# Kernel optimization log

Hardware: AMD Instinct MI355X
Metric: run time of the kernel (lower is better)

Reference implementation:

```python
import jax, jax.numpy as jnp
import numpy as np

B, S, D_MODEL, H = 4, 1024, 1024, 16
HD = D_MODEL // H  # head_dim = 64


def setup_inputs() -> dict:
    key = jax.random.key(0)
    ks = jax.random.split(key, 12)
    sd = 1.0 / np.sqrt(D_MODEL)
    return {
        "x": jax.random.normal(ks[0], (B, S, D_MODEL), dtype=jnp.float32),
        "Wq": jax.random.normal(ks[1], (D_MODEL, D_MODEL), dtype=jnp.float32) * sd,
        "bq": jnp.zeros((D_MODEL,), dtype=jnp.float32),
        "Wk": jax.random.normal(ks[2], (D_MODEL, D_MODEL), dtype=jnp.float32) * sd,
        "bk": jnp.zeros((D_MODEL,), dtype=jnp.float32),
        "Wv": jax.random.normal(ks[3], (D_MODEL, D_MODEL), dtype=jnp.float32) * sd,
        "bv": jnp.zeros((D_MODEL,), dtype=jnp.float32),
        "W1": jax.random.normal(ks[4], (2 * D_MODEL, D_MODEL), dtype=jnp.float32) * sd,
        "b1": jnp.zeros((2 * D_MODEL,), dtype=jnp.float32),
        "W2": jax.random.normal(ks[5], (D_MODEL, 2 * D_MODEL), dtype=jnp.float32) * (1.0 / np.sqrt(2 * D_MODEL)),
        "b2": jnp.zeros((D_MODEL,), dtype=jnp.float32),
        "mask": jnp.ones((B, S, S), dtype=jnp.int32),
    }


def reference(x, Wq, bq, Wk, bk, Wv, bv, W1, b1, W2, b2, mask):
    # QKV projections (torch Linear: y = x @ W.T + b), split into heads -> [B,H,S,HD]
    def proj(W, b):
        return (x @ W.T + b).reshape(B, S, H, HD).transpose(0, 2, 1, 3)

    q = proj(Wq, bq)
    k = proj(Wk, bk)
    v = proj(Wv, bv)

    scores = jnp.einsum("bhqd,bhkd->bhqk", q, k) / jnp.sqrt(jnp.float32(HD))
    # mask [B,S,S] broadcast over heads (original does unsqueeze(1).repeat)
    scores = jnp.where(mask[:, None, :, :] == 0, jnp.float32(-1e8), scores)
    probs = jax.nn.softmax(scores, axis=-1)
    ctx = jnp.einsum("bhqk,bhkd->bhqd", probs, v)
    ctx = ctx.transpose(0, 2, 1, 3).reshape(B, S, D_MODEL)

    # out-projection MLP: Linear(d, 2d) -> ReLU -> Linear(2d, d)
    h = jax.nn.relu(ctx @ W1.T + b1)
    return h @ W2.T + b2
```

## Files before the change

### kernel.cpp

```cpp
#include <hip/hip_runtime.h>
#include <hip/hip_bf16.h>
#include <stdint.h>


#define B_ 4
#define S_ 1024
#define DM_ 1024
#define H_ 16
#define HD_ 64

typedef __attribute__((ext_vector_type(8))) short short8;
typedef __attribute__((ext_vector_type(4))) float f32x4;
typedef __attribute__((ext_vector_type(4))) unsigned short ushort4v;

#define GLB_AS(p) ((const __attribute__((address_space(1))) void*)(p))
#define LDS_AS(p) ((__attribute__((address_space(3))) void*)(p))

__device__ __forceinline__ void async_load16(const void* g, void* l) {
  __builtin_amdgcn_global_load_lds(GLB_AS(g), LDS_AS(l), 16, 0, 0);
}

__device__ __forceinline__ unsigned short f2bf(float x) {
  union { float f; unsigned int u; } v; v.f = x;
  unsigned int r = v.u + 0x7fffu + ((v.u >> 16) & 1u);
  return (unsigned short)(r >> 16);
}

#define QSCALE 0.18033688011112042f

struct PrepArgs {
  const float* src[6];
  unsigned short* dst[6];
  int n4[6];
  const int* mask;
  unsigned long long* bits;
  unsigned int* rowflag;
  const float* bq;
  const float* bk;
  const float* bv;
  float* cb;
};

__global__ void prep_kernel(PrepArgs a) {
  const int seg = blockIdx.y;
  if (seg < 6) {
    const int n4 = a.n4[seg];
    const f32x4* __restrict__ src = (const f32x4*)a.src[seg];
    ushort4v* __restrict__ dst = (ushort4v*)a.dst[seg];
    for (int i = blockIdx.x * blockDim.x + threadIdx.x; i < n4;
         i += gridDim.x * blockDim.x) {
      f32x4 v = src[i];
      ushort4v o;
      o[0] = f2bf(v[0]); o[1] = f2bf(v[1]); o[2] = f2bf(v[2]); o[3] = f2bf(v[3]);
      dst[i] = o;
    }
  } else if (seg == 6) {
    const int wave = threadIdx.x >> 6;
    const int lane = threadIdx.x & 63;
    const int row = blockIdx.x * 4 + wave;
    const int4* mr = (const int4*)(a.mask + (size_t)row * S_) + lane * 4;
    unsigned int chunk = 0;
#pragma unroll
    for (int t = 0; t < 4; ++t) {
      const int4 v = mr[t];
      chunk |= (v.x != 0 ? 1u : 0u) << (4 * t + 0);
      chunk |= (v.y != 0 ? 1u : 0u) << (4 * t + 1);
      chunk |= (v.z != 0 ? 1u : 0u) << (4 * t + 2);
      chunk |= (v.w != 0 ? 1u : 0u) << (4 * t + 3);
    }
    unsigned long long v64 = (unsigned long long)chunk << (16 * (lane & 3));
    v64 |= __shfl_xor(v64, 1);
    v64 |= __shfl_xor(v64, 2);
    if ((lane & 3) == 0) a.bits[(size_t)row * 16 + (lane >> 2)] = v64;
    const bool all1 = (__ballot(chunk == 0xffffu) == ~0ull);
    if (lane == 0) a.rowflag[row] = all1 ? 1u : 0u;
  } else {
    const int i = blockIdx.x * 256 + threadIdx.x;
    if (i < 3072) {
      const float* src = (i < 1024) ? a.bq : (i < 2048) ? a.bk : a.bv;
      a.cb[i] = src[i & 1023];
    }
  }
}

enum { EPI_QKV = 0, EPI_RELU_BF16 = 2, EPI_F32 = 3, EPI_PARTIAL = 4 };

template <int EPI>
__global__ __launch_bounds__(256, 3) void gemm_bt(
    const unsigned short* __restrict__ A, const unsigned short* __restrict__ Bt,
    const float* __restrict__ bias, void* __restrict__ Cp,
    unsigned short* __restrict__ Vt, int M, int N, int K, int Kld) {
  __shared__ __align__(16) unsigned short smem[128 * 136];
  unsigned short* sA = smem;
  unsigned short* sB = smem + 128 * 64;

  const int tid = threadIdx.x;
  const int lane = tid & 63;
  const int wave = tid >> 6;
  const int quad = lane >> 4;
  const int l15 = lane & 15;
  const int swzb = l15 & 7;
  const int m0 = blockIdx.y * 128;
  const int n0 = blockIdx.x * 128;
  const int wm = (wave >> 1) * 64;
  const int wn = (wave & 1) * 64;
  const int kz = blockIdx.z * K;

  f32x4 acc[4][4];
#pragma unroll
  for (int i = 0; i < 4; ++i)
#pragma unroll
    for (int j = 0; j < 4; ++j) acc[i][j] = (f32x4){0.f, 0.f, 0.f, 0.f};

  const int srow = tid >> 3;
  const int scol = ((tid & 7) ^ (srow & 7)) * 8;
  const unsigned short* gA = A + (size_t)(m0 + srow) * Kld + kz + scol;
  const unsigned short* gB = Bt + (size_t)(n0 + srow) * Kld + kz + scol;
  unsigned short* lA = sA + tid * 8;
  unsigned short* lB = sB + tid * 8;

  for (int k0 = 0; k0 < K; k0 += 64) {
    __syncthreads();
#pragma unroll
    for (int st = 0; st < 4; ++st) {
      async_load16(gA + (size_t)(st * 32) * Kld + k0, lA + st * 2048);
      async_load16(gB + (size_t)(st * 32) * Kld + k0, lB + st * 2048);
    }
    __syncthreads();

#pragma unroll
    for (int ks = 0; ks < 2; ++ks) {
      short8 af[4], bfr[4];
#pragma unroll
      for (int t = 0; t < 4; ++t) {
        const int cg = ((ks * 4 + quad) ^ swzb) * 8;
        af[t] = *(const short8*)(sA + (wm + t * 16 + l15) * 64 + cg);
        bfr[t] = *(const short8*)(sB + (wn + t * 16 + l15) * 64 + cg);
      }
#pragma unroll
      for (int mt = 0; mt < 4; ++mt)
#pragma unroll
        for (int nt = 0; nt < 4; ++nt)
          acc[mt][nt] = __builtin_amdgcn_mfma_f32_16x16x32_bf16(
              af[mt], bfr[nt], acc[mt][nt], 0, 0, 0);
    }
  }

  if (EPI == EPI_QKV && n0 >= 2048) {
    __syncthreads();
#pragma unroll
    for (int nt = 0; nt < 4; ++nt) {
      const int col = n0 + wn + nt * 16 + l15;
      const float bv = bias[col];
#pragma unroll
      for (int mt = 0; mt < 4; ++mt)
#pragma unroll
        for (int r = 0; r < 4; ++r)
          smem[(wn + nt * 16 + l15) * 136 + wm + mt * 16 + quad * 4 + r] =
              f2bf(acc[mt][nt][r] + bv);
    }
    __syncthreads();
    const int vc0 = n0 - 2048;
    const int bb = m0 >> 10;
    const int s0 = m0 & 1023;
#pragma unroll
    for (int i = 0; i < 8; ++i) {
      const int c = i * 16 + (tid >> 4);
      const int tc = tid & 15;
      const short8 val = *(const short8*)(smem + c * 136 + tc * 8);
      const int ch = vc0 + c;
      const int hh = ch >> 6, dd = ch & 63;
      *(short8*)(Vt + ((size_t)(bb * 16 + hh) * HD_ + dd) * S_ + s0 + tc * 8) =
          val;
    }
    return;
  }

#pragma unroll
  for (int nt = 0; nt < 4; ++nt) {
    const int col = n0 + wn + nt * 16 + l15;
    const float bv = (EPI == EPI_PARTIAL) ? 0.f : bias[col];
    const float scl = (EPI == EPI_QKV && col < 1024) ? QSCALE : 1.0f;
#pragma unroll
    for (int mt = 0; mt < 4; ++mt) {
#pragma unroll
      for (int r = 0; r < 4; ++r) {
        const int row = m0 + wm + mt * 16 + quad * 4 + r;
        float v = acc[mt][nt][r] + bv;
        if (EPI == EPI_F32) {
          ((float*)Cp)[(size_t)row * N + col] = v;
        } else if (EPI == EPI_PARTIAL) {
          ((float*)Cp)[(size_t)blockIdx.z * M * N + (size_t)row * N + col] = v;
        } else if (EPI == EPI_RELU_BF16) {
          ((unsigned short*)Cp)[(size_t)row * N + col] = f2bf(fmaxf(v, 0.f));
        } else {
          ((unsigned short*)Cp)[(size_t)row * N + col] = f2bf(v * scl);
        }
      }
    }
  }
}

__global__ __launch_bounds__(256, 3) void flash_attn(
    const unsigned short* __restrict__ Cqkv, const unsigned short* __restrict__ Vt,
    const unsigned long long* __restrict__ mbits,
    const unsigned int* __restrict__ mrowflag,
    unsigned short* __restrict__ ctx) {
  __shared__ unsigned short sK[128 * 64];
  __shared__ unsigned short sV[64 * 128];
  __shared__ unsigned short spb[4][16 * 136];

  const int tid = threadIdx.x;
  const int wave = tid >> 6;
  const int lane = tid & 63;
  const int quad = lane >> 4;
  const int l15 = lane & 15;
  const int bh = blockIdx.x;
  const int b = bh >> 4;
  const int h = bh & 15;
  const int qbase = blockIdx.y * 128 + wave * 32;

  const unsigned short* Qb = Cqkv + (size_t)(b * S_) * 3072 + h * HD_;
  const unsigned short* Kb = Cqkv + (size_t)(b * S_) * 3072 + DM_ + h * HD_;
  const unsigned short* Vb = Vt + (size_t)bh * HD_ * S_;
  unsigned short* pbuf = spb[wave];

  bool mask_all_ones;
  {
    unsigned int f = mrowflag[b * S_ + qbase + (lane & 31)];
    mask_all_ones = (__ballot(f != 0) == ~0ull);
  }

  short8 qf[2][2];
#pragma unroll
  for (int u = 0; u < 2; ++u)
#pragma unroll
    for (int ks = 0; ks < 2; ++ks)
      qf[u][ks] = *(const short8*)(Qb + (size_t)(qbase + u * 16 + l15) * 3072 +
                                   ks * 32 + quad * 8);

  f32x4 o[2][4];
#pragma unroll
  for (int u = 0; u < 2; ++u)
#pragma unroll
    for (int i = 0; i < 4; ++i) o[u][i] = (f32x4){0.f, 0.f, 0.f, 0.f};
  float lsum[2][4] = {{0.f, 0.f, 0.f, 0.f}, {0.f, 0.f, 0.f, 0.f}};

  for (int kt = 0; kt < S_ / 128; ++kt) {
    const int kbase = kt * 128;

    __syncthreads();
#pragma unroll
    for (int st = 0; st < 4; ++st) {
      const int j = st * 256 + tid;
      const int r = j >> 3, c = j & 7;
      async_load16(Kb + (size_t)(kbase + r) * 3072 + ((c ^ (r & 7)) * 8),
                   sK + j * 8);
    }
#pragma unroll
    for (int st = 0; st < 4; ++st) {
      const int j = st * 256 + tid;
      const int d = j >> 4, c = j & 15;
      async_load16(Vb + (size_t)d * S_ + kbase + ((c ^ (d & 15)) * 8),
                   sV + j * 8);
    }
    __syncthreads();

    f32x4 s[2][8];
#pragma unroll
    for (int u = 0; u < 2; ++u)
#pragma unroll
      for (int i = 0; i < 8; ++i) s[u][i] = (f32x4){0.f, 0.f, 0.f, 0.f};
#pragma unroll
    for (int ks = 0; ks < 2; ++ks) {
      const int cg = ks * 4 + quad;
#pragma unroll
      for (int nt = 0; nt < 8; ++nt) {
        const int row = nt * 16 + l15;
        const short8 kf =
            *(const short8*)(sK + row * 64 + ((cg ^ (row & 7)) * 8));
        s[0][nt] = __builtin_amdgcn_mfma_f32_16x16x32_bf16(qf[0][ks], kf,
                                                           s[0][nt], 0, 0, 0);
        s[1][nt] = __builtin_amdgcn_mfma_f32_16x16x32_bf16(qf[1][ks], kf,
                                                           s[1][nt], 0, 0, 0);
      }
    }

    if (!mask_all_ones) {
#pragma unroll
      for (int u = 0; u < 2; ++u)
#pragma unroll
        for (int r = 0; r < 4; ++r) {
          const int q = qbase + u * 16 + quad * 4 + r;
          const unsigned long long* wp =
              mbits + ((size_t)(b * S_ + q)) * 16 + kt * 2;
          const unsigned long long w0 = wp[0], w1 = wp[1];
#pragma unroll
          for (int nt = 0; nt < 8; ++nt) {
            const unsigned long long w = (nt < 4) ? w0 : w1;
            const int bit = (nt * 16 + l15) & 63;
            if (!((w >> bit) & 1)) s[u][nt][r] = -1.0e8f;
          }
        }
    }

#pragma unroll
    for (int u = 0; u < 2; ++u) {
#pragma unroll
      for (int nt = 0; nt < 8; ++nt)
#pragma unroll
        for (int r = 0; r < 4; ++r) {
          const float p = __builtin_amdgcn_exp2f(s[u][nt][r]);
          lsum[u][r] += p;
          pbuf[(quad * 4 + r) * 136 + nt * 16 + l15] = f2bf(p);
        }
#pragma unroll
      for (int ks2 = 0; ks2 < 4; ++ks2) {
        const short8 pf =
            *(const short8*)(pbuf + l15 * 136 + ks2 * 32 + quad * 8);
        const int cg = ks2 * 4 + quad;
#pragma unroll
        for (int nt = 0; nt < 4; ++nt) {
          const int d = nt * 16 + l15;
          const short8 vf =
              *(const short8*)(sV + d * 128 + ((cg ^ (d & 15)) * 8));
          o[u][nt] =
              __builtin_amdgcn_mfma_f32_16x16x32_bf16(pf, vf, o[u][nt], 0, 0, 0);
        }
      }
    }
  }

#pragma unroll
  for (int u = 0; u < 2; ++u)
#pragma unroll
    for (int r = 0; r < 4; ++r) {
      float lr = lsum[u][r];
      lr += __shfl_xor(lr, 1);
      lr += __shfl_xor(lr, 2);
      lr += __shfl_xor(lr, 4);
      lr += __shfl_xor(lr, 8);
      const float inv = 1.0f / lr;
#pragma unroll
      for (int nt = 0; nt < 4; ++nt)
        pbuf[(u * 16 + quad * 4 + r) * 68 + nt * 16 + l15] =
            f2bf(o[u][nt][r] * inv);
    }
#pragma unroll
  for (int i = 0; i < 4; ++i) {
    const int j = i * 64 + lane;
    const int r = j >> 3, c = j & 7;
    const short8 val = *(const short8*)(pbuf + r * 68 + c * 8);
    *(short8*)(ctx + ((size_t)b * S_ + qbase + r) * DM_ + h * HD_ + c * 8) = val;
  }
}

__global__ void reduce_ffn2_kernel(const float* __restrict__ part,
                                   const float* __restrict__ b2,
                                   float* __restrict__ out) {
  const int i = blockIdx.x * 256 + threadIdx.x;
  const f32x4 a = ((const f32x4*)part)[i];
  const f32x4 b = ((const f32x4*)part)[i + (B_ * S_ * DM_ / 4)];
  const f32x4 bb = ((const f32x4*)b2)[i & 255];
  ((f32x4*)out)[i] = a + b + bb;
}

extern "C" void kernel_launch(void* const* d_in, const int* in_sizes, int n_in,
                              void* d_out, int out_size, void* d_ws,
                              size_t ws_size, hipStream_t stream) {
  const float* x = (const float*)d_in[0];
  const float* Wq = (const float*)d_in[1];
  const float* bq = (const float*)d_in[2];
  const float* Wk = (const float*)d_in[3];
  const float* bk = (const float*)d_in[4];
  const float* Wv = (const float*)d_in[5];
  const float* bv = (const float*)d_in[6];
  const float* W1 = (const float*)d_in[7];
  const float* b1 = (const float*)d_in[8];
  const float* W2 = (const float*)d_in[9];
  const float* b2 = (const float*)d_in[10];
  const int* mask = (const int*)d_in[11];
  float* out = (float*)d_out;

  char* ws = (char*)d_ws;
  unsigned short* xb   = (unsigned short*)(ws + 0);
  unsigned short* wqkv = (unsigned short*)(ws + 8388608);
  unsigned short* w1b  = (unsigned short*)(ws + 14680064);
  unsigned short* w2b  = (unsigned short*)(ws + 18874368);
  unsigned short* Cqkv = (unsigned short*)(ws + 23068672);
  unsigned short* ctxb = (unsigned short*)(ws + 48234496);
  unsigned short* hb   = (unsigned short*)(ws + 56623104);
  unsigned short* Vt   = (unsigned short*)(ws + 56623104);
  unsigned long long* mbits = (unsigned long long*)(ws + 73400320);
  unsigned int* mrowflag    = (unsigned int*)(ws + 73924608);
  float* cb                 = (float*)(ws + 73940992);
  float* part = (float*)(ws + 23068672);

  PrepArgs pa;
  pa.src[0] = x;  pa.dst[0] = xb;               pa.n4[0] = (B_ * S_ * DM_) / 4;
  pa.src[1] = Wq; pa.dst[1] = wqkv;             pa.n4[1] = (DM_ * DM_) / 4;
  pa.src[2] = Wk; pa.dst[2] = wqkv + DM_ * DM_; pa.n4[2] = (DM_ * DM_) / 4;
  pa.src[3] = Wv; pa.dst[3] = wqkv + 2 * DM_ * DM_; pa.n4[3] = (DM_ * DM_) / 4;
  pa.src[4] = W1; pa.dst[4] = w1b;              pa.n4[4] = (2 * DM_ * DM_) / 4;
  pa.src[5] = W2; pa.dst[5] = w2b;              pa.n4[5] = (2 * DM_ * DM_) / 4;
  pa.mask = mask; pa.bits = mbits; pa.rowflag = mrowflag;
  pa.bq = bq; pa.bk = bk; pa.bv = bv; pa.cb = cb;
  prep_kernel<<<dim3(1024, 8), 256, 0, stream>>>(pa);

  const int M = B_ * S_;
  gemm_bt<EPI_QKV><<<dim3(3 * DM_ / 128, M / 128), 256, 0, stream>>>(
      xb, wqkv, cb, Cqkv, Vt, M, 3 * DM_, DM_, DM_);

  flash_attn<<<dim3(B_ * H_, S_ / 128), 256, 0, stream>>>(
      Cqkv, Vt, mbits, mrowflag, ctxb);

  gemm_bt<EPI_RELU_BF16><<<dim3((2 * DM_) / 128, M / 128), 256, 0, stream>>>(
      ctxb, w1b, b1, hb, nullptr, M, 2 * DM_, DM_, DM_);

  gemm_bt<EPI_PARTIAL><<<dim3(DM_ / 128, M / 128, 2), 256, 0, stream>>>(
      hb, w2b, b2, part, nullptr, M, DM_, DM_, 2 * DM_);
  reduce_ffn2_kernel<<<dim3(M * DM_ / 4 / 256), 256, 0, stream>>>(part, b2, out);
}
```

Before: 247.9 us.

## Fuse FFN2 split-K reduction into a 512-thread block and batch attention PV MFMAs

Replaces the two-way split-K FFN2 GEMM plus separate reduction kernel with one 512-thread block per tile. Each half computes one K half, and the two are summed through LDS before the bias is added and fp32 output is written. This removes the partial-buffer round trip through global memory and one kernel launch. The flash attention kernel now writes both 16-row P sub-tiles to a larger LDS buffer and interleaves the PV MFMAs, so each V fragment load is reused twice. Occupancy for flash_attn is lowered from 3 to 2 blocks per unit to make room for the extra LDS, and the FFN2 grid now has half as many workgroups.

```diff
diff --git a/kernel.cpp b/kernel.cpp
--- a/kernel.cpp
+++ b/kernel.cpp
@@ -83,7 +83,7 @@
   }
 }
 
-enum { EPI_QKV = 0, EPI_RELU_BF16 = 2, EPI_F32 = 3, EPI_PARTIAL = 4 };
+enum { EPI_QKV = 0, EPI_RELU_BF16 = 2 };
 
 template <int EPI>
 __global__ __launch_bounds__(256, 3) void gemm_bt(
@@ -104,7 +104,6 @@
   const int n0 = blockIdx.x * 128;
   const int wm = (wave >> 1) * 64;
   const int wn = (wave & 1) * 64;
-  const int kz = blockIdx.z * K;
 
   f32x4 acc[4][4];
 #pragma unroll
@@ -114,8 +113,8 @@
 
   const int srow = tid >> 3;
   const int scol = ((tid & 7) ^ (srow & 7)) * 8;
-  const unsigned short* gA = A + (size_t)(m0 + srow) * Kld + kz + scol;
-  const unsigned short* gB = Bt + (size_t)(n0 + srow) * Kld + kz + scol;
+  const unsigned short* gA = A + (size_t)(m0 + srow) * Kld + scol;
+  const unsigned short* gB = Bt + (size_t)(n0 + srow) * Kld + scol;
   unsigned short* lA = sA + tid * 8;
   unsigned short* lB = sB + tid * 8;
 
@@ -179,7 +178,7 @@
 #pragma unroll
   for (int nt = 0; nt < 4; ++nt) {
     const int col = n0 + wn + nt * 16 + l15;
-    const float bv = (EPI == EPI_PARTIAL) ? 0.f : bias[col];
+    const float bv = bias[col];
     const float scl = (EPI == EPI_QKV && col < 1024) ? QSCALE : 1.0f;
 #pragma unroll
     for (int mt = 0; mt < 4; ++mt) {
@@ -187,11 +186,7 @@
       for (int r = 0; r < 4; ++r) {
         const int row = m0 + wm + mt * 16 + quad * 4 + r;
         float v = acc[mt][nt][r] + bv;
-        if (EPI == EPI_F32) {
-          ((float*)Cp)[(size_t)row * N + col] = v;
-        } else if (EPI == EPI_PARTIAL) {
-          ((float*)Cp)[(size_t)blockIdx.z * M * N + (size_t)row * N + col] = v;
-        } else if (EPI == EPI_RELU_BF16) {
+        if (EPI == EPI_RELU_BF16) {
           ((unsigned short*)Cp)[(size_t)row * N + col] = f2bf(fmaxf(v, 0.f));
         } else {
           ((unsigned short*)Cp)[(size_t)row * N + col] = f2bf(v * scl);
@@ -201,14 +196,108 @@
   }
 }
 
-__global__ __launch_bounds__(256, 3) void flash_attn(
+__global__ __launch_bounds__(512, 1) void gemm_ffn2(
+    const unsigned short* __restrict__ A, const unsigned short* __restrict__ Bt,
+    const float* __restrict__ bias, float* __restrict__ out) {
+  __shared__ __align__(16) unsigned short smem[4 * 128 * 64];
+  const int tid512 = threadIdx.x;
+  const int half = tid512 >> 8;
+  const int tid = tid512 & 255;
+  unsigned short* sA = smem + half * 2 * 128 * 64;
+  unsigned short* sB = sA + 128 * 64;
+
+  const int lane = tid & 63;
+  const int wave = tid >> 6;
+  const int quad = lane >> 4;
+  const int l15 = lane & 15;
+  const int swzb = l15 & 7;
+  const int m0 = blockIdx.y * 128;
+  const int n0 = blockIdx.x * 128;
+  const int wm = (wave >> 1) * 64;
+  const int wn = (wave & 1) * 64;
+  const int kz = half * 1024;
+
+  f32x4 acc[4][4];
+#pragma unroll
+  for (int i = 0; i < 4; ++i)
+#pragma unroll
+    for (int j = 0; j < 4; ++j) acc[i][j] = (f32x4){0.f, 0.f, 0.f, 0.f};
+
+  const int srow = tid >> 3;
+  const int scol = ((tid & 7) ^ (srow & 7)) * 8;
+  const unsigned short* gA = A + (size_t)(m0 + srow) * 2048 + kz + scol;
+  const unsigned short* gB = Bt + (size_t)(n0 + srow) * 2048 + kz + scol;
+  unsigned short* lA = sA + tid * 8;
+  unsigned short* lB = sB + tid * 8;
+
+  for (int k0 = 0; k0 < 1024; k0 += 64) {
+    __syncthreads();
+#pragma unroll
+    for (int st = 0; st < 4; ++st) {
+      async_load16(gA + (size_t)(st * 32) * 2048 + k0, lA + st * 2048);
+      async_load16(gB + (size_t)(st * 32) * 2048 + k0, lB + st * 2048);
+    }
+    __syncthreads();
+
+#pragma unroll
+    for (int ks = 0; ks < 2; ++ks) {
+      short8 af[4], bfr[4];
+#pragma unroll
+      for (int t = 0; t < 4; ++t) {
+        const int cg = ((ks * 4 + quad) ^ swzb) * 8;
+        af[t] = *(const short8*)(sA + (wm + t * 16 + l15) * 64 + cg);
+        bfr[t] = *(const short8*)(sB + (wn + t * 16 + l15) * 64 + cg);
+      }
+#pragma unroll
+      for (int mt = 0; mt < 4; ++mt)
+#pragma unroll
+        for (int nt = 0; nt < 4; ++nt)
+          acc[mt][nt] = __builtin_amdgcn_mfma_f32_16x16x32_bf16(
+              af[mt], bfr[nt], acc[mt][nt], 0, 0, 0);
+    }
+  }
+
+  __syncthreads();
+  float* fbuf = (float*)smem;
+  if (half == 1) {
+#pragma unroll
+    for (int nt = 0; nt < 4; ++nt)
+#pragma unroll
+      for (int mt = 0; mt < 4; ++mt)
+#pragma unroll
+        for (int r = 0; r < 4; ++r)
+          fbuf[wave * 4096 + (mt * 16 + quad * 4 + r) * 64 + nt * 16 + l15] =
+              acc[mt][nt][r];
+  }
+  __syncthreads();
+  if (half == 0) {
+#pragma unroll
+    for (int nt = 0; nt < 4; ++nt) {
+      const int col = n0 + wn + nt * 16 + l15;
+      const float bv = bias[col];
+#pragma unroll
+      for (int mt = 0; mt < 4; ++mt)
+#pragma unroll
+        for (int r = 0; r < 4; ++r) {
+          const int row = m0 + wm + mt * 16 + quad * 4 + r;
+          const float v =
+              acc[mt][nt][r] +
+              fbuf[wave * 4096 + (mt * 16 + quad * 4 + r) * 64 + nt * 16 + l15] +
+              bv;
+          out[(size_t)row * DM_ + col] = v;
+        }
+    }
+  }
+}
+
+__global__ __launch_bounds__(256, 2) void flash_attn(
     const unsigned short* __restrict__ Cqkv, const unsigned short* __restrict__ Vt,
     const unsigned long long* __restrict__ mbits,
     const unsigned int* __restrict__ mrowflag,
     unsigned short* __restrict__ ctx) {
   __shared__ unsigned short sK[128 * 64];
   __shared__ unsigned short sV[64 * 128];
-  __shared__ unsigned short spb[4][16 * 136];
+  __shared__ unsigned short spb[4][32 * 136];
 
   const int tid = threadIdx.x;
   const int wave = tid >> 6;
@@ -305,28 +394,30 @@
     }
 
 #pragma unroll
-    for (int u = 0; u < 2; ++u) {
+    for (int u = 0; u < 2; ++u)
 #pragma unroll
       for (int nt = 0; nt < 8; ++nt)
 #pragma unroll
         for (int r = 0; r < 4; ++r) {
           const float p = __builtin_amdgcn_exp2f(s[u][nt][r]);
           lsum[u][r] += p;
-          pbuf[(quad * 4 + r) * 136 + nt * 16 + l15] = f2bf(p);
+          pbuf[(u * 16 + quad * 4 + r) * 136 + nt * 16 + l15] = f2bf(p);
         }
-#pragma unroll
-      for (int ks2 = 0; ks2 < 4; ++ks2) {
-        const short8 pf =
-            *(const short8*)(pbuf + l15 * 136 + ks2 * 32 + quad * 8);
-        const int cg = ks2 * 4 + quad;
-#pragma unroll
-        for (int nt = 0; nt < 4; ++nt) {
-          const int d = nt * 16 + l15;
-          const short8 vf =
-              *(const short8*)(sV + d * 128 + ((cg ^ (d & 15)) * 8));
-          o[u][nt] =
-              __builtin_amdgcn_mfma_f32_16x16x32_bf16(pf, vf, o[u][nt], 0, 0, 0);
-        }
+
+#pragma unroll
+    for (int ks2 = 0; ks2 < 4; ++ks2) {
+      const short8 pf0 =
+          *(const short8*)(pbuf + l15 * 136 + ks2 * 32 + quad * 8);
+      const short8 pf1 =
+          *(const short8*)(pbuf + (16 + l15) * 136 + ks2 * 32 + quad * 8);
+      const int cg = ks2 * 4 + quad;
+#pragma unroll
+      for (int nt = 0; nt < 4; ++nt) {
+        const int d = nt * 16 + l15;
+        const short8 vf =
+            *(const short8*)(sV + d * 128 + ((cg ^ (d & 15)) * 8));
+        o[0][nt] = __builtin_amdgcn_mfma_f32_16x16x32_bf16(pf0, vf, o[0][nt], 0, 0, 0);
+        o[1][nt] = __builtin_amdgcn_mfma_f32_16x16x32_bf16(pf1, vf, o[1][nt], 0, 0, 0);
       }
     }
   }
@@ -353,16 +444,6 @@
     const short8 val = *(const short8*)(pbuf + r * 68 + c * 8);
     *(short8*)(ctx + ((size_t)b * S_ + qbase + r) * DM_ + h * HD_ + c * 8) = val;
   }
-}
-
-__global__ void reduce_ffn2_kernel(const float* __restrict__ part,
-                                   const float* __restrict__ b2,
-                                   float* __restrict__ out) {
-  const int i = blockIdx.x * 256 + threadIdx.x;
-  const f32x4 a = ((const f32x4*)part)[i];
-  const f32x4 b = ((const f32x4*)part)[i + (B_ * S_ * DM_ / 4)];
-  const f32x4 bb = ((const f32x4*)b2)[i & 255];
-  ((f32x4*)out)[i] = a + b + bb;
 }
 
 extern "C" void kernel_launch(void* const* d_in, const int* in_sizes, int n_in,
@@ -394,7 +475,6 @@
   unsigned long long* mbits = (unsigned long long*)(ws + 73400320);
   unsigned int* mrowflag    = (unsigned int*)(ws + 73924608);
   float* cb                 = (float*)(ws + 73940992);
-  float* part = (float*)(ws + 23068672);
 
   PrepArgs pa;
   pa.src[0] = x;  pa.dst[0] = xb;               pa.n4[0] = (B_ * S_ * DM_) / 4;
@@ -417,7 +497,5 @@
   gemm_bt<EPI_RELU_BF16><<<dim3((2 * DM_) / 128, M / 128), 256, 0, stream>>>(
       ctxb, w1b, b1, hb, nullptr, M, 2 * DM_, DM_, DM_);
 
-  gemm_bt<EPI_PARTIAL><<<dim3(DM_ / 128, M / 128, 2), 256, 0, stream>>>(
-      hb, w2b, b2, part, nullptr, M, DM_, DM_, 2 * DM_);
-  reduce_ffn2_kernel<<<dim3(M * DM_ / 4 / 256), 256, 0, stream>>>(part, b2, out);
-}
+  gemm_ffn2<<<dim3(DM_ / 128, M / 128), 512, 0, stream>>>(hb, w2b, b2, out);
+}
```

Result: faster. 231.2 us (-6.8%).
